# Optimization experiments

Measured on AMD Instinct MI355X. Metric: run time of the kernel, lower is better.

Reference implementation:

```python
import jax, jax.numpy as jnp
import numpy as np

N_NODES = 100000
D_IN = 256
D_OUT = 128
N_EDGES = 1600000


def setup_inputs() -> dict:
    key = jax.random.key(0)
    k1, k2, k3, k4 = jax.random.split(key, 4)
    x = jax.random.normal(k1, (N_NODES, D_IN), dtype=jnp.float32)
    edge_index = jax.random.randint(k2, (2, N_EDGES), 0, N_NODES, dtype=jnp.int64)
    # GCNConv parameters (glorot-style scale)
    W = jax.random.normal(k3, (D_IN, D_OUT), dtype=jnp.float32) * (1.0 / np.sqrt(D_IN))
    b = jax.random.normal(k4, (D_OUT,), dtype=jnp.float32) * 0.01
    return {"x": x, "edge_index": edge_index, "W": W, "b": b}


def reference(x, edge_index, W, b):
    n = x.shape[0]
    # add self-loops (PyG GCNConv default)
    loop = jnp.arange(n, dtype=edge_index.dtype)
    src = jnp.concatenate([edge_index[0], loop])
    dst = jnp.concatenate([edge_index[1], loop])
    # symmetric normalization: deg^-1/2[src] * deg^-1/2[dst]
    ones = jnp.ones(src.shape[0], dtype=x.dtype)
    deg = jax.ops.segment_sum(ones, dst, num_segments=n)
    dinv = jnp.where(deg > 0, jax.lax.rsqrt(deg), 0.0)
    norm = dinv[src] * dinv[dst]  # [E+N]
    # linear transform at nodes, then gather-scale-scatter over edges
    h = x @ W  # [N, d_out]
    msg = h[src] * norm[:, None]  # [E+N, d_out]
    out = jax.ops.segment_sum(msg, dst, num_segments=n) + b
    # CRD.forward: relu then dropout (identity in eval mode)
    return jax.nn.relu(out)
```

## Files before the change

kernel.cpp:

```cpp
#include <hip/hip_runtime.h>
#include <stdint.h>

#define D_IN 256
#define D_OUT 128
#define MAXB 800
#define NCHUNK 256

typedef __attribute__((ext_vector_type(8))) short bf16x8;
typedef __attribute__((ext_vector_type(4))) float f32x4;

__device__ __forceinline__ unsigned short f2bf(float f) {
  union { float f; uint32_t u; } v; v.f = f;
  uint32_t u = v.u;
  uint32_t r = (u + 0x7FFFu + ((u >> 16) & 1u)) >> 16;
  return (unsigned short)r;
}
__device__ __forceinline__ float bf_lo(uint32_t u) {
  union { uint32_t u; float f; } v; v.u = u << 16; return v.f;
}
__device__ __forceinline__ float bf_hi(uint32_t u) {
  union { uint32_t u; float f; } v; v.u = u & 0xFFFF0000u; return v.f;
}

__device__ __forceinline__ void dma16(const float* gsrc, float* ldst) {
  __builtin_amdgcn_global_load_lds(
      (const __attribute__((address_space(1))) void*)gsrc,
      (__attribute__((address_space(3))) void*)ldst, 16, 0, 0);
}

__global__ __launch_bounds__(256) void k_conv_w(const float* __restrict__ W,
                                                unsigned short* __restrict__ wt) {
  int idx = blockIdx.x * 256 + threadIdx.x;
  int n = idx >> 8;
  int k = idx & 255;
  wt[idx] = f2bf(W[k * D_OUT + n]);
}

__global__ __launch_bounds__(512) void k_gemm(const float* __restrict__ x,
                                              const unsigned short* __restrict__ wt,
                                              unsigned short* __restrict__ hp, int N) {
  __shared__ float xl[2][16][256];

  int wave = threadIdx.x >> 6;
  int lane = threadIdx.x & 63;
  int m = lane & 15;
  int q = lane >> 4;

  bf16x8 bw[8];
  const unsigned short* wrow = wt + (size_t)(wave * 16 + m) * D_IN + q * 8;
#pragma unroll
  for (int kt = 0; kt < 8; ++kt)
    bw[kt] = *reinterpret_cast<const bf16x8*>(wrow + kt * 32);

  int tiles = (N + 15) >> 4;
  int ipb = (tiles + gridDim.x - 1) / gridDim.x;
  int t0 = blockIdx.x * ipb;
  int tend = t0 + ipb;
  if (tend > tiles) tend = tiles;
  if (t0 >= tend) return;

  auto stage_tile = [&](int buf, int tt) {
#pragma unroll
    for (int rr = 0; rr < 2; ++rr) {
      int r = wave + rr * 8;
      const float* gsrc = x + ((size_t)tt * 16 + r) * D_IN + ((lane ^ (r & 7)) << 2);
      dma16(gsrc, &xl[buf][r][0]);
    }
  };

  stage_tile(0, t0);
  __syncthreads();

  int cur = 0;
  int sw = m & 7;

  for (int t = t0; t < tend; ++t) {
    if (t + 1 < tend) stage_tile(cur ^ 1, t + 1);

    const float* prow = &xl[cur][m][0];
    f32x4 acc = {0.f, 0.f, 0.f, 0.f};
#pragma unroll
    for (int kt = 0; kt < 8; ++kt) {
      int g0 = q * 2 + kt * 8;
      float4 u0 = *reinterpret_cast<const float4*>(prow + ((g0 ^ sw) << 2));
      float4 u1 = *reinterpret_cast<const float4*>(prow + (((g0 + 1) ^ sw) << 2));
      bf16x8 av;
      av[0] = (short)f2bf(u0.x); av[1] = (short)f2bf(u0.y);
      av[2] = (short)f2bf(u0.z); av[3] = (short)f2bf(u0.w);
      av[4] = (short)f2bf(u1.x); av[5] = (short)f2bf(u1.y);
      av[6] = (short)f2bf(u1.z); av[7] = (short)f2bf(u1.w);
      acc = __builtin_amdgcn_mfma_f32_16x16x32_bf16(av, bw[kt], acc, 0, 0, 0);
    }

    int r0 = t * 16;
#pragma unroll
    for (int r = 0; r < 4; ++r) {
      int row = r0 + q * 4 + r;
      hp[(size_t)row * D_OUT + wave * 16 + m] = f2bf(acc[r]);
    }

    __syncthreads();
    cur ^= 1;
  }
}

__global__ __launch_bounds__(256) void k_passA(const int* __restrict__ ei, int E, int CH,
                                               int NB, int* __restrict__ cntm) {
  __shared__ int bins[MAXB];
  int c = blockIdx.x;
  for (int b = threadIdx.x; b < NB; b += 256) bins[b] = 0;
  __syncthreads();
  int start = c * CH, end = min(E, start + CH);
  for (int eb = start + (int)threadIdx.x * 4; eb < end; eb += 1024) {
    int kmax = end - eb; if (kmax > 4) kmax = 4;
    if (kmax == 4) {
      int4 v = *reinterpret_cast<const int4*>(ei + E + eb);
      atomicAdd(&bins[v.x >> 7], 1);
      atomicAdd(&bins[v.y >> 7], 1);
      atomicAdd(&bins[v.z >> 7], 1);
      atomicAdd(&bins[v.w >> 7], 1);
    } else {
      for (int k = 0; k < kmax; ++k) atomicAdd(&bins[ei[E + eb + k] >> 7], 1);
    }
  }
  __syncthreads();
  for (int b = threadIdx.x; b < NB; b += 256) cntm[(size_t)b * NCHUNK + c] = bins[b];
}

__global__ __launch_bounds__(NCHUNK) void k_scanB1(const int* __restrict__ cntm,
                                                   int* __restrict__ ofs,
                                                   int* __restrict__ tot) {
  __shared__ int sc[NCHUNK];
  int b = blockIdx.x, t = threadIdx.x;
  int v = cntm[(size_t)b * NCHUNK + t];
  sc[t] = v;
  __syncthreads();
  for (int off = 1; off < NCHUNK; off <<= 1) {
    int val = (t >= off) ? sc[t - off] : 0;
    __syncthreads();
    sc[t] += val;
    __syncthreads();
  }
  ofs[(size_t)b * NCHUNK + t] = sc[t] - v;
  if (t == NCHUNK - 1) tot[b] = sc[t];
}

__global__ __launch_bounds__(256) void k_scanB2(const int* __restrict__ tot,
                                                int* __restrict__ base, int NB,
                                                int* __restrict__ nptr, int N, int E) {
  __shared__ int sc[256];
  int t = threadIdx.x;
  int v[4];
  int s = 0;
#pragma unroll
  for (int j = 0; j < 4; ++j) {
    int i = t * 4 + j;
    v[j] = (i < NB) ? tot[i] : 0;
    s += v[j];
  }
  sc[t] = s;
  __syncthreads();
  for (int off = 1; off < 256; off <<= 1) {
    int val = (t >= off) ? sc[t - off] : 0;
    __syncthreads();
    sc[t] += val;
    __syncthreads();
  }
  int ex = sc[t] - s;
#pragma unroll
  for (int j = 0; j < 4; ++j) {
    int i = t * 4 + j;
    if (i < NB) base[i] = ex;
    ex += v[j];
  }
  if (t == 0) nptr[N] = E;
}

__global__ __launch_bounds__(256) void k_passC(const int* __restrict__ ei, int E, int CH,
                                               int NB, const int* __restrict__ ofs,
                                               const int* __restrict__ base,
                                               int* __restrict__ P) {
  __shared__ int cur[MAXB];
  int c = blockIdx.x;
  for (int b = threadIdx.x; b < NB; b += 256)
    cur[b] = base[b] + ofs[(size_t)b * NCHUNK + c];
  __syncthreads();
  int start = c * CH, end = min(E, start + CH);
  for (int eb = start + (int)threadIdx.x * 4; eb < end; eb += 1024) {
    int kmax = end - eb; if (kmax > 4) kmax = 4;
    int s4[4], d4[4];
    if (kmax == 4) {
      int4 vs = *reinterpret_cast<const int4*>(ei + eb);
      int4 vd = *reinterpret_cast<const int4*>(ei + E + eb);
      s4[0] = vs.x; s4[1] = vs.y; s4[2] = vs.z; s4[3] = vs.w;
      d4[0] = vd.x; d4[1] = vd.y; d4[2] = vd.z; d4[3] = vd.w;
    } else {
      for (int k = 0; k < kmax; ++k) { s4[k] = ei[eb + k]; d4[k] = ei[E + eb + k]; }
    }
#pragma unroll
    for (int k = 0; k < 4; ++k) {
      if (k >= kmax) break;
      int d = d4[k];
      int p = atomicAdd(&cur[d >> 7], 1);
      P[p] = s4[k] | ((d & 127) << 17);
    }
  }
}

__global__ __launch_bounds__(256) void k_sortd(const int* __restrict__ P,
                                               const int* __restrict__ base,
                                               const int* __restrict__ tot,
                                               int* __restrict__ nptr,
                                               float* __restrict__ dinv,
                                               int* __restrict__ P2, int N) {
  __shared__ int ideg[128];
  __shared__ int sc[128];
  __shared__ int cur[128];
  int b = blockIdx.x, t = threadIdx.x;
  if (t < 128) ideg[t] = 0;
  __syncthreads();
  int s0 = base[b], T = tot[b];
  for (int i = s0 + t; i < s0 + T; i += 256) atomicAdd(&ideg[P[i] >> 17], 1);
  __syncthreads();
  if (t < 128) sc[t] = ideg[t];
  __syncthreads();
  for (int off = 1; off < 128; off <<= 1) {
    int v = (t < 128 && t >= off) ? sc[t - off] : 0;
    __syncthreads();
    if (t < 128) sc[t] += v;
    __syncthreads();
  }
  if (t < 128) {
    int exc = s0 + sc[t] - ideg[t];
    int node = b * 128 + t;
    if (node < N) {
      nptr[node] = exc;
      dinv[node] = rsqrtf(1.0f + (float)ideg[t]);
    }
    cur[t] = exc;
  }
  __syncthreads();
  for (int i = s0 + t; i < s0 + T; i += 256) {
    int pk = P[i];
    int p = atomicAdd(&cur[pk >> 17], 1);
    P2[p] = pk & 0x1FFFF;
  }
}

__global__ __launch_bounds__(256) void k_agg(const int* __restrict__ P2,
                                             const int* __restrict__ nptr,
                                             const uint4* __restrict__ hrows,
                                             const float* __restrict__ dinv,
                                             const float* __restrict__ bias,
                                             float* __restrict__ out, int N) {
  int wave = threadIdx.x >> 6, lane = threadIdx.x & 63;
  int node = blockIdx.x * 4 + wave;
  if (node >= N) return;
  int rs = nptr[node], re = nptr[node + 1];
  int j = lane >> 4, c = lane & 15;

  float acc[8];
#pragma unroll
  for (int k = 0; k < 8; ++k) acc[k] = 0.f;

  for (int e = rs + j; e < re; e += 4) {
    int src = P2[e];
    float r = dinv[src];
    uint4 u = hrows[(size_t)src * 16 + c];
    acc[0] += r * bf_lo(u.x); acc[1] += r * bf_hi(u.x);
    acc[2] += r * bf_lo(u.y); acc[3] += r * bf_hi(u.y);
    acc[4] += r * bf_lo(u.z); acc[5] += r * bf_hi(u.z);
    acc[6] += r * bf_lo(u.w); acc[7] += r * bf_hi(u.w);
  }
#pragma unroll
  for (int k = 0; k < 8; ++k) {
    acc[k] += __shfl_xor(acc[k], 16);
    acc[k] += __shfl_xor(acc[k], 32);
  }
  if (j == 0) {
    float rsn = dinv[node];
    uint4 uh = hrows[(size_t)node * 16 + c];
    float self[8] = {bf_lo(uh.x), bf_hi(uh.x), bf_lo(uh.y), bf_hi(uh.y),
                     bf_lo(uh.z), bf_hi(uh.z), bf_lo(uh.w), bf_hi(uh.w)};
    const float4* b4 = reinterpret_cast<const float4*>(bias);
    float4 b0 = b4[c * 2], b1 = b4[c * 2 + 1];
    float bb[8] = {b0.x, b0.y, b0.z, b0.w, b1.x, b1.y, b1.z, b1.w};
    float o[8];
#pragma unroll
    for (int k = 0; k < 8; ++k) {
      float v = rsn * (acc[k] + rsn * self[k]) + bb[k];
      o[k] = v > 0.f ? v : 0.f;
    }
    float4* orow = reinterpret_cast<float4*>(out + (size_t)node * D_OUT + c * 8);
    orow[0] = float4{o[0], o[1], o[2], o[3]};
    orow[1] = float4{o[4], o[5], o[6], o[7]};
  }
}

extern "C" void kernel_launch(void* const* d_in, const int* in_sizes, int n_in,
                              void* d_out, int out_size, void* d_ws, size_t ws_size,
                              hipStream_t stream) {
  const float* x = (const float*)d_in[0];
  const int* ei = (const int*)d_in[1];
  const float* W = (const float*)d_in[2];
  const float* bias = (const float*)d_in[3];
  int N = in_sizes[0] / D_IN;
  int E = in_sizes[1] / 2;
  float* out = (float*)d_out;

  int NB = (N + 127) >> 7;
  int CH = ((E + NCHUNK - 1) / NCHUNK + 3) & ~3;

  char* w = (char*)d_ws;
  size_t off = 0;
  auto alloc = [&](size_t bytes) -> void* {
    void* p = w + off;
    off = (off + bytes + 255) & ~(size_t)255;
    return p;
  };
  unsigned short* wt = (unsigned short*)alloc((size_t)D_IN * D_OUT * 2);
  unsigned short* hp = (unsigned short*)alloc((size_t)N * D_OUT * 2);
  float* dinv = (float*)alloc((size_t)N * 4);
  int* cntm = (int*)alloc((size_t)NB * NCHUNK * 4);
  int* ofs = (int*)alloc((size_t)NB * NCHUNK * 4);
  int* tot = (int*)alloc((size_t)NB * 4);
  int* base = (int*)alloc((size_t)NB * 4);
  int* nptr = (int*)alloc((size_t)(N + 1) * 4);
  int* P = (int*)alloc((size_t)E * 4);
  int* P2 = (int*)alloc((size_t)E * 4);
  (void)ws_size; (void)n_in; (void)out_size;

  int tiles = (N + 15) >> 4;
  int gblocks = tiles < 1024 ? tiles : 1024;

  k_conv_w<<<(D_IN * D_OUT) / 256, 256, 0, stream>>>(W, wt);
  k_gemm<<<gblocks, 512, 0, stream>>>(x, wt, hp, N);
  k_passA<<<NCHUNK, 256, 0, stream>>>(ei, E, CH, NB, cntm);
  k_scanB1<<<NB, NCHUNK, 0, stream>>>(cntm, ofs, tot);
  k_scanB2<<<1, 256, 0, stream>>>(tot, base, NB, nptr, N, E);
  k_passC<<<NCHUNK, 256, 0, stream>>>(ei, E, CH, NB, ofs, base, P);
  k_sortd<<<NB, 256, 0, stream>>>(P, base, tot, nptr, dinv, P2, N);
  k_agg<<<(N + 3) / 4, 256, 0, stream>>>(P2, nptr, (const uint4*)hp, dinv, bias, out, N);
}
```

Baseline: 304.1 us.

## Prescale GEMM rows by dinv and unroll aggregation gather by two

The GEMM now runs after the degree/sort stage and multiplies each output row by dinv[src] before bf16 rounding. The aggregation kernel therefore drops the per-edge dinv[src] load and multiply. Its edge loop is also unrolled to issue two row gathers per iteration, which gives more loads in flight. The trade-offs are a serialised launch order, since the GEMM can no longer be independent of the sort stage, and slightly different bf16 rounding of the scaled values.

```diff
diff --git a/kernel.cpp b/kernel.cpp
--- a/kernel.cpp
+++ b/kernel.cpp
@@ -38,6 +38,7 @@
 
 __global__ __launch_bounds__(512) void k_gemm(const float* __restrict__ x,
                                               const unsigned short* __restrict__ wt,
+                                              const float* __restrict__ dinv,
                                               unsigned short* __restrict__ hp, int N) {
   __shared__ float xl[2][16][256];
 
@@ -96,7 +97,7 @@
 #pragma unroll
     for (int r = 0; r < 4; ++r) {
       int row = r0 + q * 4 + r;
-      hp[(size_t)row * D_OUT + wave * 16 + m] = f2bf(acc[r]);
+      hp[(size_t)row * D_OUT + wave * 16 + m] = f2bf(dinv[row] * acc[r]);
     }
 
     __syncthreads();
@@ -263,14 +264,28 @@
 #pragma unroll
   for (int k = 0; k < 8; ++k) acc[k] = 0.f;
 
-  for (int e = rs + j; e < re; e += 4) {
-    int src = P2[e];
-    float r = dinv[src];
-    uint4 u = hrows[(size_t)src * 16 + c];
-    acc[0] += r * bf_lo(u.x); acc[1] += r * bf_hi(u.x);
-    acc[2] += r * bf_lo(u.y); acc[3] += r * bf_hi(u.y);
-    acc[4] += r * bf_lo(u.z); acc[5] += r * bf_hi(u.z);
-    acc[6] += r * bf_lo(u.w); acc[7] += r * bf_hi(u.w);
+  int e = rs + j;
+  for (; e + 4 < re; e += 8) {
+    int s0 = P2[e];
+    int s1 = P2[e + 4];
+    uint4 u0 = hrows[(size_t)s0 * 16 + c];
+    uint4 u1 = hrows[(size_t)s1 * 16 + c];
+    acc[0] += bf_lo(u0.x) + bf_lo(u1.x);
+    acc[1] += bf_hi(u0.x) + bf_hi(u1.x);
+    acc[2] += bf_lo(u0.y) + bf_lo(u1.y);
+    acc[3] += bf_hi(u0.y) + bf_hi(u1.y);
+    acc[4] += bf_lo(u0.z) + bf_lo(u1.z);
+    acc[5] += bf_hi(u0.z) + bf_hi(u1.z);
+    acc[6] += bf_lo(u0.w) + bf_lo(u1.w);
+    acc[7] += bf_hi(u0.w) + bf_hi(u1.w);
+  }
+  if (e < re) {
+    int s0 = P2[e];
+    uint4 u0 = hrows[(size_t)s0 * 16 + c];
+    acc[0] += bf_lo(u0.x); acc[1] += bf_hi(u0.x);
+    acc[2] += bf_lo(u0.y); acc[3] += bf_hi(u0.y);
+    acc[4] += bf_lo(u0.z); acc[5] += bf_hi(u0.z);
+    acc[6] += bf_lo(u0.w); acc[7] += bf_hi(u0.w);
   }
 #pragma unroll
   for (int k = 0; k < 8; ++k) {
@@ -288,7 +303,7 @@
     float o[8];
 #pragma unroll
     for (int k = 0; k < 8; ++k) {
-      float v = rsn * (acc[k] + rsn * self[k]) + bb[k];
+      float v = rsn * (acc[k] + self[k]) + bb[k];
       o[k] = v > 0.f ? v : 0.f;
     }
     float4* orow = reinterpret_cast<float4*>(out + (size_t)node * D_OUT + c * 8);
@@ -334,11 +349,11 @@
   int gblocks = tiles < 1024 ? tiles : 1024;
 
   k_conv_w<<<(D_IN * D_OUT) / 256, 256, 0, stream>>>(W, wt);
-  k_gemm<<<gblocks, 512, 0, stream>>>(x, wt, hp, N);
   k_passA<<<NCHUNK, 256, 0, stream>>>(ei, E, CH, NB, cntm);
   k_scanB1<<<NB, NCHUNK, 0, stream>>>(cntm, ofs, tot);
   k_scanB2<<<1, 256, 0, stream>>>(tot, base, NB, nptr, N, E);
   k_passC<<<NCHUNK, 256, 0, stream>>>(ei, E, CH, NB, ofs, base, P);
   k_sortd<<<NB, 256, 0, stream>>>(P, base, tot, nptr, dinv, P2, N);
+  k_gemm<<<gblocks, 512, 0, stream>>>(x, wt, dinv, hp, N);
   k_agg<<<(N + 3) / 4, 256, 0, stream>>>(P2, nptr, (const uint4*)hp, dinv, bias, out, N);
 }
```

After: 300.8 us. No clear change (-1.1%).
